# Performance work log

Hardware: AMD Instinct MI355X
Metric: run time of the kernel (lower is better)

The kernel has to match this reference:

```python
import jax, jax.numpy as jnp
import numpy as np

N = 8192
IN_F = 512
OUT_F = 64
NEG_SLOPE = 0.01  # nn.LeakyReLU default
MASK_VAL = -1e9


def setup_inputs() -> dict:
    key = jax.random.key(0)
    k_h, k_adj, k_W, k_a = jax.random.split(key, 4)
    h = jax.random.normal(k_h, (N, IN_F), dtype=jnp.float32)
    adjacency = jax.random.randint(k_adj, (N, N), 0, 2, dtype=jnp.int32)
    # xavier_uniform bounds
    bW = float(np.sqrt(6.0 / (IN_F + OUT_F)))
    ba = float(np.sqrt(6.0 / (2 * OUT_F + 1)))
    W = jax.random.uniform(k_W, (IN_F, OUT_F), minval=-bW, maxval=bW, dtype=jnp.float32)
    a = jax.random.uniform(k_a, (2 * OUT_F, 1), minval=-ba, maxval=ba, dtype=jnp.float32)
    return {"h": h, "adjacency": adjacency, "W": W, "a": a}


def reference(h, adjacency, W, a):
    WH = h @ W                                  # [N, out_f]
    wh1 = WH @ a[:OUT_F, :]                     # [N, 1]
    wh2 = WH @ a[OUT_F:, :]                     # [N, 1]
    e = jax.nn.leaky_relu(wh1 + wh2.T, negative_slope=NEG_SLOPE)  # [N, N]
    attnt = jnp.where(adjacency > 0, e, jnp.float32(MASK_VAL))
    attnt = jax.nn.softmax(attnt, axis=1)       # row-wise softmax
    hfirst = attnt @ WH                         # [N, out_f]
    return jax.nn.elu(hfirst)
```

## Files before the change

kernel.cpp:

```cpp
#include <hip/hip_runtime.h>
#include <hip/hip_bf16.h>

#define N 8192
#define IN_F 512
#define OUT_F 64
#define S_SPLIT 8
#define JT (N / S_SPLIT)

typedef __attribute__((ext_vector_type(8))) short short8;
typedef __attribute__((ext_vector_type(4))) float floatx4;
typedef __attribute__((ext_vector_type(4))) int intx4;

__device__ inline short f2bf(float x) {
    __hip_bfloat16 b = __float2bfloat16(x);
    return __builtin_bit_cast(short, b);
}

__global__ void k_wt(const float* __restrict__ W, short* __restrict__ WT) {
    int idx = blockIdx.x * 256 + threadIdx.x;
    int k = idx >> 6, f = idx & 63;
    WT[f * IN_F + k] = f2bf(W[k * OUT_F + f]);
}

__global__ __launch_bounds__(256) void k_wh(const float* __restrict__ h,
                                            const short* __restrict__ WT,
                                            float* __restrict__ WH,
                                            short* __restrict__ WHbT) {
    int w = threadIdx.x >> 6;
    int lane = threadIdx.x & 63;
    int n = lane & 15, q = lane >> 4;
    int i0 = blockIdx.x * 64 + w * 16;
    int rowA = i0 + n;
    const float* hp = h + (size_t)rowA * IN_F + q * 8;
    floatx4 acc[4] = {};
    for (int k0 = 0; k0 < IN_F; k0 += 32) {
        floatx4 h0 = *(const floatx4*)(hp + k0);
        floatx4 h1 = *(const floatx4*)(hp + k0 + 4);
        short8 af;
#pragma unroll
        for (int j = 0; j < 4; j++) { af[j] = f2bf(h0[j]); af[j + 4] = f2bf(h1[j]); }
#pragma unroll
        for (int b = 0; b < 4; b++) {
            short8 bf_ = *(const short8*)(WT + (b * 16 + n) * IN_F + k0 + q * 8);
            acc[b] = __builtin_amdgcn_mfma_f32_16x16x32_bf16(af, bf_, acc[b], 0, 0, 0);
        }
    }
#pragma unroll
    for (int b = 0; b < 4; b++) {
#pragma unroll
        for (int r = 0; r < 4; r++) {
            int row = i0 + q * 4 + r;
            int col = b * 16 + n;
            float v = acc[b][r];
            WH[row * OUT_F + col] = v;
            WHbT[(size_t)col * N + row] = f2bf(v);
        }
    }
}

__global__ void k_wh12(const float* __restrict__ WH, const float* __restrict__ a,
                       float* __restrict__ wh1, float* __restrict__ wh2) {
    int row = blockIdx.x * 256 + threadIdx.x;
    float s1 = 0.f, s2 = 0.f;
#pragma unroll 8
    for (int f = 0; f < OUT_F; f++) {
        float v = WH[row * OUT_F + f];
        s1 += v * a[f];
        s2 += v * a[OUT_F + f];
    }
    wh1[row] = s1;
    wh2[row] = s2;
}

__global__ __launch_bounds__(256) void k_attn(const int* __restrict__ adj,
                                              const short* __restrict__ WHbT,
                                              const float* __restrict__ wh1,
                                              const float* __restrict__ wh2,
                                              float* __restrict__ num,
                                              float* __restrict__ den) {
    int w = threadIdx.x >> 6;
    int lane = threadIdx.x & 63;
    int n = lane & 15, q = lane >> 4;
    int i0 = blockIdx.x * 64 + w * 16;
    int rowA = i0 + n;
    int j0 = blockIdx.y * JT;

    const int* ap = adj + (size_t)rowA * N + j0 + q * 8;
    const float* w2p = wh2 + j0 + q * 8;
    const short* bp0 = WHbT + (size_t)n * N + j0 + q * 8;
    float my_wh1 = wh1[rowA];

    floatx4 acc[4] = {};
    float dsum = 0.f;

    for (int t = 0; t < JT; t += 32) {
        intx4 a0 = *(const intx4*)(ap);
        intx4 a1 = *(const intx4*)(ap + 4);
        floatx4 w20 = *(const floatx4*)(w2p);
        floatx4 w21 = *(const floatx4*)(w2p + 4);
        ap += 32;
        w2p += 32;
        float p[8];
#pragma unroll
        for (int jj = 0; jj < 8; jj++) {
            int av = (jj < 4) ? a0[jj] : a1[jj - 4];
            float e = my_wh1 + ((jj < 4) ? w20[jj] : w21[jj - 4]);
            float el = fmaxf(e, 0.01f * e);
            float pv = __expf(el);
            pv = (av > 0) ? pv : 0.f;
            p[jj] = pv;
            dsum += pv;
        }
        short8 af;
#pragma unroll
        for (int jj = 0; jj < 8; jj++) af[jj] = f2bf(p[jj]);
#pragma unroll
        for (int b = 0; b < 4; b++) {
            short8 bf_ = *(const short8*)(bp0 + (size_t)b * 16 * N + t);
            acc[b] = __builtin_amdgcn_mfma_f32_16x16x32_bf16(af, bf_, acc[b], 0, 0, 0);
        }
    }

    dsum += __shfl_xor(dsum, 16, 64);
    dsum += __shfl_xor(dsum, 32, 64);
    if (q == 0) atomicAdd(&den[rowA], dsum);

#pragma unroll
    for (int b = 0; b < 4; b++) {
#pragma unroll
        for (int r = 0; r < 4; r++) {
            int row = i0 + q * 4 + r;
            atomicAdd(&num[row * OUT_F + b * 16 + n], acc[b][r]);
        }
    }
}

__global__ void k_final(const float* __restrict__ num, const float* __restrict__ den,
                        float* __restrict__ out) {
    int idx = blockIdx.x * 256 + threadIdx.x;
    int row = idx >> 6;
    float x = num[idx] / den[row];
    out[idx] = (x > 0.f) ? x : (__expf(x) - 1.f);
}

extern "C" void kernel_launch(void* const* d_in, const int* in_sizes, int n_in,
                              void* d_out, int out_size, void* d_ws, size_t ws_size,
                              hipStream_t stream) {
    const float* h = (const float*)d_in[0];
    const int* adj = (const int*)d_in[1];
    const float* W = (const float*)d_in[2];
    const float* a = (const float*)d_in[3];
    float* out = (float*)d_out;

    char* ws = (char*)d_ws;
    float* WH   = (float*)(ws);
    short* WHbT = (short*)(ws + (size_t)(2 << 20));
    short* WT   = (short*)(ws + (size_t)(3 << 20));
    float* wh1  = (float*)(ws + (size_t)(3 << 20) + (64 << 10));
    float* wh2  = wh1 + N;
    float* num  = (float*)(ws + (size_t)(4 << 20));
    float* den  = (float*)(ws + (size_t)(6 << 20));

    hipMemsetAsync(ws + (size_t)(4 << 20), 0, (size_t)(2 << 20) + N * sizeof(float), stream);

    k_wt<<<dim3(128), dim3(256), 0, stream>>>(W, WT);
    k_wh<<<dim3(128), dim3(256), 0, stream>>>(h, WT, WH, WHbT);
    k_wh12<<<dim3(N / 256), dim3(256), 0, stream>>>(WH, a, wh1, wh2);
    k_attn<<<dim3(128, S_SPLIT), dim3(256), 0, stream>>>(adj, WHbT, wh1, wh2, num, den);
    k_final<<<dim3((N * OUT_F) / 256), dim3(256), 0, stream>>>(num, den, out);
}
```

Baseline: 447.0 us.

## Split attention wider, prefetch adjacency, replace atomics with partial buffers, transpose WH via LDS

The attention kernel now uses 16 column splits instead of 8 and an occupancy hint in its launch bounds. It software-prefetches the next adjacency and wh2 chunk while computing the current one, and hoists the B-operand loads ahead of the exp math. Atomic accumulation of numerator and denominator is replaced by per-split partial buffers that the final kernel reduces, which removes the memset and atomic contention but adds 32MB of partial writes and reads. The WH projection kernel is regridded to 64-thread blocks and transposes its output through shared memory, so the bf16 transposed writes become vectorized.

```diff
diff --git a/kernel.cpp b/kernel.cpp
--- a/kernel.cpp
+++ b/kernel.cpp
@@ -4,7 +4,7 @@
 #define N 8192
 #define IN_F 512
 #define OUT_F 64
-#define S_SPLIT 8
+#define S_SPLIT 16
 #define JT (N / S_SPLIT)
 
 typedef __attribute__((ext_vector_type(8))) short short8;
@@ -22,14 +22,14 @@
     WT[f * IN_F + k] = f2bf(W[k * OUT_F + f]);
 }
 
-__global__ __launch_bounds__(256) void k_wh(const float* __restrict__ h,
-                                            const short* __restrict__ WT,
-                                            float* __restrict__ WH,
-                                            short* __restrict__ WHbT) {
-    int w = threadIdx.x >> 6;
-    int lane = threadIdx.x & 63;
+__global__ __launch_bounds__(64) void k_wh(const float* __restrict__ h,
+                                           const short* __restrict__ WT,
+                                           float* __restrict__ WH,
+                                           short* __restrict__ WHbT) {
+    __shared__ float tile[OUT_F][17];
+    int lane = threadIdx.x;
     int n = lane & 15, q = lane >> 4;
-    int i0 = blockIdx.x * 64 + w * 16;
+    int i0 = blockIdx.x * 16;
     int rowA = i0 + n;
     const float* hp = h + (size_t)rowA * IN_F + q * 8;
     floatx4 acc[4] = {};
@@ -49,13 +49,20 @@
     for (int b = 0; b < 4; b++) {
 #pragma unroll
         for (int r = 0; r < 4; r++) {
-            int row = i0 + q * 4 + r;
+            int rl = q * 4 + r;
             int col = b * 16 + n;
             float v = acc[b][r];
-            WH[row * OUT_F + col] = v;
-            WHbT[(size_t)col * N + row] = f2bf(v);
+            WH[(i0 + rl) * OUT_F + col] = v;
+            tile[col][rl] = v;
         }
     }
+    __syncthreads();
+    const float* tc = tile[lane];
+    short8 s0, s1;
+#pragma unroll
+    for (int k = 0; k < 8; k++) { s0[k] = f2bf(tc[k]); s1[k] = f2bf(tc[k + 8]); }
+    *(short8*)(WHbT + (size_t)lane * N + i0) = s0;
+    *(short8*)(WHbT + (size_t)lane * N + i0 + 8) = s1;
 }
 
 __global__ void k_wh12(const float* __restrict__ WH, const float* __restrict__ a,
@@ -72,18 +79,19 @@
     wh2[row] = s2;
 }
 
-__global__ __launch_bounds__(256) void k_attn(const int* __restrict__ adj,
-                                              const short* __restrict__ WHbT,
-                                              const float* __restrict__ wh1,
-                                              const float* __restrict__ wh2,
-                                              float* __restrict__ num,
-                                              float* __restrict__ den) {
+__global__ __launch_bounds__(256, 6) void k_attn(const int* __restrict__ adj,
+                                                 const short* __restrict__ WHbT,
+                                                 const float* __restrict__ wh1,
+                                                 const float* __restrict__ wh2,
+                                                 float* __restrict__ num_part,
+                                                 float* __restrict__ den_part) {
     int w = threadIdx.x >> 6;
     int lane = threadIdx.x & 63;
     int n = lane & 15, q = lane >> 4;
     int i0 = blockIdx.x * 64 + w * 16;
     int rowA = i0 + n;
-    int j0 = blockIdx.y * JT;
+    int split = blockIdx.y;
+    int j0 = split * JT;
 
     const int* ap = adj + (size_t)rowA * N + j0 + q * 8;
     const float* w2p = wh2 + j0 + q * 8;
@@ -93,18 +101,30 @@
     floatx4 acc[4] = {};
     float dsum = 0.f;
 
+    intx4 ca0 = *(const intx4*)(ap);
+    intx4 ca1 = *(const intx4*)(ap + 4);
+    floatx4 cw0 = *(const floatx4*)(w2p);
+    floatx4 cw1 = *(const floatx4*)(w2p + 4);
+
     for (int t = 0; t < JT; t += 32) {
-        intx4 a0 = *(const intx4*)(ap);
-        intx4 a1 = *(const intx4*)(ap + 4);
-        floatx4 w20 = *(const floatx4*)(w2p);
-        floatx4 w21 = *(const floatx4*)(w2p + 4);
-        ap += 32;
-        w2p += 32;
+        intx4 na0 = ca0, na1 = ca1;
+        floatx4 nw0 = cw0, nw1 = cw1;
+        if (t + 32 < JT) {
+            na0 = *(const intx4*)(ap + 32);
+            na1 = *(const intx4*)(ap + 36);
+            nw0 = *(const floatx4*)(w2p + 32);
+            nw1 = *(const floatx4*)(w2p + 36);
+        }
+        short8 bfr[4];
+#pragma unroll
+        for (int b = 0; b < 4; b++)
+            bfr[b] = *(const short8*)(bp0 + (size_t)b * 16 * N + t);
+
         float p[8];
 #pragma unroll
         for (int jj = 0; jj < 8; jj++) {
-            int av = (jj < 4) ? a0[jj] : a1[jj - 4];
-            float e = my_wh1 + ((jj < 4) ? w20[jj] : w21[jj - 4]);
+            int av = (jj < 4) ? ca0[jj] : ca1[jj - 4];
+            float e = my_wh1 + ((jj < 4) ? cw0[jj] : cw1[jj - 4]);
             float el = fmaxf(e, 0.01f * e);
             float pv = __expf(el);
             pv = (av > 0) ? pv : 0.f;
@@ -115,31 +135,37 @@
 #pragma unroll
         for (int jj = 0; jj < 8; jj++) af[jj] = f2bf(p[jj]);
 #pragma unroll
-        for (int b = 0; b < 4; b++) {
-            short8 bf_ = *(const short8*)(bp0 + (size_t)b * 16 * N + t);
-            acc[b] = __builtin_amdgcn_mfma_f32_16x16x32_bf16(af, bf_, acc[b], 0, 0, 0);
-        }
+        for (int b = 0; b < 4; b++)
+            acc[b] = __builtin_amdgcn_mfma_f32_16x16x32_bf16(af, bfr[b], acc[b], 0, 0, 0);
+
+        ap += 32; w2p += 32;
+        ca0 = na0; ca1 = na1; cw0 = nw0; cw1 = nw1;
     }
 
     dsum += __shfl_xor(dsum, 16, 64);
     dsum += __shfl_xor(dsum, 32, 64);
-    if (q == 0) atomicAdd(&den[rowA], dsum);
+    if (q == 0) den_part[(size_t)split * N + rowA] = dsum;
 
+    float* np_ = num_part + (size_t)split * N * OUT_F;
 #pragma unroll
-    for (int b = 0; b < 4; b++) {
+    for (int b = 0; b < 4; b++)
 #pragma unroll
-        for (int r = 0; r < 4; r++) {
-            int row = i0 + q * 4 + r;
-            atomicAdd(&num[row * OUT_F + b * 16 + n], acc[b][r]);
-        }
-    }
+        for (int r = 0; r < 4; r++)
+            np_[(i0 + q * 4 + r) * OUT_F + b * 16 + n] = acc[b][r];
 }
 
-__global__ void k_final(const float* __restrict__ num, const float* __restrict__ den,
+__global__ void k_final(const float* __restrict__ num_part,
+                        const float* __restrict__ den_part,
                         float* __restrict__ out) {
     int idx = blockIdx.x * 256 + threadIdx.x;
     int row = idx >> 6;
-    float x = num[idx] / den[row];
+    float s = 0.f, d = 0.f;
+#pragma unroll
+    for (int sp = 0; sp < S_SPLIT; sp++) {
+        s += num_part[(size_t)sp * N * OUT_F + idx];
+        d += den_part[sp * N + row];
+    }
+    float x = s / d;
     out[idx] = (x > 0.f) ? x : (__expf(x) - 1.f);
 }
 
@@ -153,19 +179,17 @@
     float* out = (float*)d_out;
 
     char* ws = (char*)d_ws;
-    float* WH   = (float*)(ws);
-    short* WHbT = (short*)(ws + (size_t)(2 << 20));
-    short* WT   = (short*)(ws + (size_t)(3 << 20));
-    float* wh1  = (float*)(ws + (size_t)(3 << 20) + (64 << 10));
-    float* wh2  = wh1 + N;
-    float* num  = (float*)(ws + (size_t)(4 << 20));
-    float* den  = (float*)(ws + (size_t)(6 << 20));
-
-    hipMemsetAsync(ws + (size_t)(4 << 20), 0, (size_t)(2 << 20) + N * sizeof(float), stream);
+    float* WH    = (float*)(ws);
+    short* WHbT  = (short*)(ws + (size_t)(2 << 20));
+    short* WT    = (short*)(ws + (size_t)(3 << 20));
+    float* wh1   = (float*)(ws + (size_t)(3 << 20) + (64 << 10));
+    float* wh2   = wh1 + N;
+    float* num_p = (float*)(ws + (size_t)(4 << 20));
+    float* den_p = (float*)(ws + (size_t)(36 << 20));
 
     k_wt<<<dim3(128), dim3(256), 0, stream>>>(W, WT);
-    k_wh<<<dim3(128), dim3(256), 0, stream>>>(h, WT, WH, WHbT);
+    k_wh<<<dim3(N / 16), dim3(64), 0, stream>>>(h, WT, WH, WHbT);
     k_wh12<<<dim3(N / 256), dim3(256), 0, stream>>>(WH, a, wh1, wh2);
-    k_attn<<<dim3(128, S_SPLIT), dim3(256), 0, stream>>>(adj, WHbT, wh1, wh2, num, den);
-    k_final<<<dim3((N * OUT_F) / 256), dim3(256), 0, stream>>>(num, den, out);
+    k_attn<<<dim3(128, S_SPLIT), dim3(256), 0, stream>>>(adj, WHbT, wh1, wh2, num_p, den_p);
+    k_final<<<dim3((N * OUT_F) / 256), dim3(256), 0, stream>>>(num_p, den_p, out);
 }
```

After: 444.5 us. About the same (-0.6%).
